# Kernel tuning notes

Measured on AMD Instinct MI355X. Metric: run time of the kernel, lower is better.

## Reference

```python
import jax, jax.numpy as jnp
import numpy as np

N_NEURONS = 256
P_MAX = 8
N_BLOCKS = P_MAX + 1
HIDDEN = 32
BATCH = 8192


def setup_inputs() -> dict:
    key = jax.random.key(0)
    ks = jax.random.split(key, 9)
    z = jax.random.normal(ks[0], (BATCH, N_BLOCKS * N_NEURONS), dtype=jnp.float32)
    # Per-block ScalarMLP params, stacked over the n_blocks axis.
    s1 = 1.0 / np.sqrt(N_NEURONS)
    s2 = 1.0 / np.sqrt(HIDDEN)
    gW1 = jax.random.uniform(ks[1], (N_BLOCKS, N_NEURONS, HIDDEN), jnp.float32, -s1, s1)
    gb1 = jax.random.uniform(ks[2], (N_BLOCKS, HIDDEN), jnp.float32, -s1, s1)
    gW2 = jax.random.uniform(ks[3], (N_BLOCKS, HIDDEN, HIDDEN), jnp.float32, -s2, s2)
    gb2 = jax.random.uniform(ks[4], (N_BLOCKS, HIDDEN), jnp.float32, -s2, s2)
    gW3 = jax.random.uniform(ks[5], (N_BLOCKS, HIDDEN), jnp.float32, -s2, s2)
    gb3 = jax.random.uniform(ks[6], (N_BLOCKS,), jnp.float32, -s2, s2)
    # Lag coupling matrices W_r ~ U(-init_scale, init_scale), init_scale=0.1
    W = jax.random.uniform(ks[7], (P_MAX, N_NEURONS, N_NEURONS), jnp.float32, -0.1, 0.1)
    return {"z": z, "gW1": gW1, "gb1": gb1, "gW2": gW2, "gb2": gb2,
            "gW3": gW3, "gb3": gb3, "W": W}


def _energy(z, gW1, gb1, gW2, gb2, gW3, gb3, W):
    B = z.shape[0]
    blocks = z.reshape(B, N_BLOCKS, N_NEURONS)           # (B, K, n)
    # Per-block ScalarMLP energies (all blocks at once).
    h1 = jax.nn.silu(jnp.einsum('bkn,knh->bkh', blocks, gW1) + gb1)   # (B, K, H)
    h2 = jax.nn.silu(jnp.einsum('bkh,khg->bkg', h1, gW2) + gb2)       # (B, K, H)
    e = jnp.einsum('bkh,kh->bk', h2, gW3) + gb3                        # (B, K)
    # Bilinear lag couplings: z_future^T W_r z_{lag-r}, r = 1..p_max.
    z_future = blocks[:, P_MAX, :]                                     # (B, n)
    lags = blocks[:, :P_MAX, :][:, ::-1, :]                            # (B, p, n), index r-1 == block p_max-r
    cross = jnp.einsum('bi,rij,brj->b', z_future, W, lags)             # (B,)
    return e.sum(axis=-1) + cross                                      # (B,)


def reference(z, gW1, gb1, gW2, gb2, gW3, gb3, W):
    # Score s(z) = -grad_z U(z); sum over batch gives per-sample grads
    # since energies are independent across samples.
    grad_z = jax.grad(lambda zz: _energy(zz, gW1, gb1, gW2, gb2, gW3, gb3, W).sum())(z)
    return -grad_z
```

## Files before the change

kernel.cpp:

```cpp
#include <hip/hip_runtime.h>
#include <hip/hip_bf16.h>
#include <math.h>

#define BATCH 8192
#define NB 9
#define NN 256
#define PMAX 8
#define HID 32
#define ZDIM 2304

typedef short bf16x8 __attribute__((ext_vector_type(8)));
typedef float f32x4 __attribute__((ext_vector_type(4)));

static __device__ inline unsigned short f2bf(float f) {
    __hip_bfloat16 h = __float2bfloat16(f);
    return *reinterpret_cast<unsigned short*>(&h);
}

static __device__ inline uint4 pack8(float4 a, float4 b) {
    uint4 u;
    u.x = (unsigned)f2bf(a.x) | ((unsigned)f2bf(a.y) << 16);
    u.y = (unsigned)f2bf(a.z) | ((unsigned)f2bf(a.w) << 16);
    u.z = (unsigned)f2bf(b.x) | ((unsigned)f2bf(b.y) << 16);
    u.w = (unsigned)f2bf(b.z) | ((unsigned)f2bf(b.w) << 16);
    return u;
}

__global__ __launch_bounds__(256) void k_pack(
    const float* __restrict__ W, const float* __restrict__ gW1,
    unsigned short* __restrict__ Wb, unsigned short* __restrict__ WTb,
    unsigned short* __restrict__ gW1b, unsigned short* __restrict__ g1Tb) {
    int r = blockIdx.z;
    int t = threadIdx.x;
    if (r < 8) {
        __shared__ float tt[32][33];
        int i0 = blockIdx.y * 32;
        int j0 = blockIdx.x * 32;
        int tx = t & 31;
        int ty = t >> 5;
        const float* src = W + (size_t)r * 65536;
        #pragma unroll
        for (int s = 0; s < 32; s += 8) {
            float v = src[(size_t)(i0 + ty + s) * 256 + (j0 + tx)];
            tt[ty + s][tx] = v;
            Wb[(size_t)r * 65536 + (size_t)(i0 + ty + s) * 256 + (j0 + tx)] = f2bf(v);
        }
        __syncthreads();
        #pragma unroll
        for (int s = 0; s < 32; s += 8)
            WTb[(size_t)r * 65536 + (size_t)(j0 + ty + s) * 256 + (i0 + tx)] = f2bf(tt[tx][ty + s]);
    } else {
        int tg = (blockIdx.y * 8 + blockIdx.x) * 256 + t;
        for (int e = tg; e < 73728; e += 16384) {
            float v = gW1[e];
            unsigned short b = f2bf(v);
            gW1b[e] = b;
            int k = e >> 13, n = (e >> 5) & 255, h = e & 31;
            g1Tb[(size_t)(k * 32 + h) * 256 + n] = b;
        }
    }
}

__global__ __launch_bounds__(256) void k_mlp(
    const float* __restrict__ z, const unsigned short* __restrict__ g1Tb,
    const float* __restrict__ gb1, const float* __restrict__ gW2,
    const float* __restrict__ gb2, const float* __restrict__ gW3,
    float* __restrict__ d1ws) {
    __shared__ uint4 As4[512];
    __shared__ uint4 Bw[1024];
    __shared__ uint4 W2Ts4[128];
    __shared__ uint4 W2Ns4[128];

    int t = threadIdx.x;
    int lane = t & 63;
    int w = t >> 6;
    int k = blockIdx.y;
    int b0 = blockIdx.x * 128;

    const unsigned short* bsrc = g1Tb + (size_t)k * 8192;
    for (int e = t; e < 1024; e += 256) {
        int h = e >> 5;
        int rest = e & 31;
        int c = rest >> 2, q = rest & 3;
        Bw[c * 128 + (h & 15) + 16 * q + 64 * (h >> 4)] =
            *(const uint4*)(bsrc + (size_t)h * 256 + c * 32 + q * 8);
    }
    const float* gw2 = gW2 + (size_t)k * 1024;
    unsigned short* w2t = (unsigned short*)W2Ts4;
    unsigned short* w2n = (unsigned short*)W2Ns4;
    for (int e = t; e < 1024; e += 256) {
        int n = e >> 5, kk = e & 31;
        int q = kk >> 3, jj = kk & 7;
        int ci = (n & 15) + 16 * q + 64 * (n >> 4);
        w2t[ci * 8 + jj] = f2bf(gw2[kk * 32 + n]);
        w2n[ci * 8 + jj] = f2bf(gw2[n * 32 + kk]);
    }

    int mq_m = t >> 2;
    int q = t & 3;

    f32x4 acc1[2][2];
    #pragma unroll
    for (int i = 0; i < 2; ++i)
        #pragma unroll
        for (int j = 0; j < 2; ++j) acc1[i][j] = (f32x4){0.f, 0.f, 0.f, 0.f};

    for (int c = 0; c < 8; ++c) {
        float4 fa[2][2];
        #pragma unroll
        for (int pp = 0; pp < 2; ++pp) {
            int m = mq_m + 64 * pp;
            const float* as = z + (size_t)(b0 + m) * ZDIM + k * 256 + c * 32 + q * 8;
            fa[pp][0] = *(const float4*)(as);
            fa[pp][1] = *(const float4*)(as + 4);
        }
        __syncthreads();
        #pragma unroll
        for (int pp = 0; pp < 2; ++pp) {
            int m = mq_m + 64 * pp;
            As4[(m & 15) + 16 * q + 64 * (m >> 4)] = pack8(fa[pp][0], fa[pp][1]);
        }
        __syncthreads();
        bf16x8 af[2], bfr[2];
        #pragma unroll
        for (int i = 0; i < 2; ++i) af[i] = __builtin_bit_cast(bf16x8, As4[lane + (w * 2 + i) * 64]);
        #pragma unroll
        for (int j = 0; j < 2; ++j) bfr[j] = __builtin_bit_cast(bf16x8, Bw[c * 128 + lane + j * 64]);
        #pragma unroll
        for (int i = 0; i < 2; ++i)
            #pragma unroll
            for (int j = 0; j < 2; ++j)
                acc1[i][j] = __builtin_amdgcn_mfma_f32_16x16x32_bf16(af[i], bfr[j], acc1[i][j], 0, 0, 0);
    }

    int cq = lane >> 4;
    int ci16 = lane & 15;
    float b1v[2], b2v[2], g3v[2];
    #pragma unroll
    for (int j = 0; j < 2; ++j) {
        b1v[j] = gb1[k * 32 + j * 16 + ci16];
        b2v[j] = gb2[k * 32 + j * 16 + ci16];
        g3v[j] = gW3[k * 32 + j * 16 + ci16];
    }
    unsigned short* Hs = (unsigned short*)As4;
    float sp1[2][2][4];
    __syncthreads();
    #pragma unroll
    for (int i = 0; i < 2; ++i)
        #pragma unroll
        for (int j = 0; j < 2; ++j)
            #pragma unroll
            for (int r = 0; r < 4; ++r) {
                float a1 = acc1[i][j][r] + b1v[j];
                float s1 = 1.f / (1.f + __expf(-a1));
                sp1[i][j][r] = s1 * (1.f + a1 * (1.f - s1));
                int row = w * 32 + i * 16 + cq * 4 + r;
                int col = j * 16 + ci16;
                int chunk = (row & 15) + 16 * (col >> 3) + 64 * (row >> 4);
                Hs[chunk * 8 + (col & 7)] = f2bf(a1 * s1);
            }
    __syncthreads();

    bf16x8 af2[2], wf[2];
    #pragma unroll
    for (int i = 0; i < 2; ++i) af2[i] = __builtin_bit_cast(bf16x8, As4[lane + (w * 2 + i) * 64]);
    #pragma unroll
    for (int j = 0; j < 2; ++j) wf[j] = __builtin_bit_cast(bf16x8, W2Ts4[lane + j * 64]);
    f32x4 acc2[2][2];
    #pragma unroll
    for (int i = 0; i < 2; ++i)
        #pragma unroll
        for (int j = 0; j < 2; ++j) {
            acc2[i][j] = (f32x4){0.f, 0.f, 0.f, 0.f};
            acc2[i][j] = __builtin_amdgcn_mfma_f32_16x16x32_bf16(af2[i], wf[j], acc2[i][j], 0, 0, 0);
        }

    __syncthreads();
    #pragma unroll
    for (int i = 0; i < 2; ++i)
        #pragma unroll
        for (int j = 0; j < 2; ++j)
            #pragma unroll
            for (int r = 0; r < 4; ++r) {
                float a2 = acc2[i][j][r] + b2v[j];
                float s2 = 1.f / (1.f + __expf(-a2));
                float da2 = g3v[j] * s2 * (1.f + a2 * (1.f - s2));
                int row = w * 32 + i * 16 + cq * 4 + r;
                int col = j * 16 + ci16;
                int chunk = (row & 15) + 16 * (col >> 3) + 64 * (row >> 4);
                Hs[chunk * 8 + (col & 7)] = f2bf(da2);
            }
    __syncthreads();

    bf16x8 af3[2], wg[2];
    #pragma unroll
    for (int i = 0; i < 2; ++i) af3[i] = __builtin_bit_cast(bf16x8, As4[lane + (w * 2 + i) * 64]);
    #pragma unroll
    for (int j = 0; j < 2; ++j) wg[j] = __builtin_bit_cast(bf16x8, W2Ns4[lane + j * 64]);
    #pragma unroll
    for (int i = 0; i < 2; ++i)
        #pragma unroll
        for (int j = 0; j < 2; ++j) {
            f32x4 a3 = (f32x4){0.f, 0.f, 0.f, 0.f};
            a3 = __builtin_amdgcn_mfma_f32_16x16x32_bf16(af3[i], wg[j], a3, 0, 0, 0);
            #pragma unroll
            for (int r = 0; r < 4; ++r) {
                int row = w * 32 + i * 16 + cq * 4 + r;
                int col = j * 16 + ci16;
                d1ws[((size_t)k * BATCH + b0 + row) * 32 + col] = a3[r] * sp1[i][j][r];
            }
        }
}

__global__ __launch_bounds__(256) void k_gemm_lo(
    const float* __restrict__ z, const float* __restrict__ d1,
    const unsigned short* __restrict__ WTb, const unsigned short* __restrict__ gW1b,
    float* __restrict__ out) {
    __shared__ uint4 As4[512];
    __shared__ uint4 Bs4[512];

    int t = threadIdx.x;
    int lane = t & 63;
    int w = t >> 6;
    int wr = w >> 1, wc = w & 1;
    int b0 = blockIdx.y * 128;
    int n0 = blockIdx.x * 128;
    int k  = n0 >> 8;
    int jb = n0 & 255;

    const float* Amain = z + (size_t)b0 * ZDIM + 2048;
    const float* Aext  = d1 + ((size_t)k * BATCH + b0) * 32;
    const unsigned short* Bmain = WTb + (size_t)(7 - k) * 65536 + (size_t)jb * 256;
    const unsigned short* Bext  = gW1b + ((size_t)k * 256 + jb) * 32;

    int mq_m = t >> 2;
    int q    = t & 3;

    f32x4 acc[4][4];
    #pragma unroll
    for (int i = 0; i < 4; ++i)
        #pragma unroll
        for (int j = 0; j < 4; ++j) acc[i][j] = (f32x4){0.f, 0.f, 0.f, 0.f};

    for (int c = 0; c < 9; ++c) {
        int kb = c * 32;
        float4 fa[2][2];
        uint4 bu[2];
        #pragma unroll
        for (int pp = 0; pp < 2; ++pp) {
            int m = mq_m + 64 * pp;
            const float* as = (c < 8) ? (Amain + (size_t)m * ZDIM + kb + q * 8)
                                      : (Aext + (size_t)m * 32 + q * 8);
            fa[pp][0] = *(const float4*)(as);
            fa[pp][1] = *(const float4*)(as + 4);
            const unsigned short* bs = (c < 8) ? (Bmain + (size_t)m * 256 + kb + q * 8)
                                               : (Bext + (size_t)m * 32 + q * 8);
            bu[pp] = *(const uint4*)(bs);
        }
        __syncthreads();
        #pragma unroll
        for (int pp = 0; pp < 2; ++pp) {
            int m = mq_m + 64 * pp;
            int ci = (m & 15) + 16 * q + 64 * (m >> 4);
            As4[ci] = pack8(fa[pp][0], fa[pp][1]);
            Bs4[ci] = bu[pp];
        }
        __syncthreads();
        bf16x8 af[4], bf[4];
        #pragma unroll
        for (int i = 0; i < 4; ++i) af[i] = __builtin_bit_cast(bf16x8, As4[lane + (wr * 4 + i) * 64]);
        #pragma unroll
        for (int j = 0; j < 4; ++j) bf[j] = __builtin_bit_cast(bf16x8, Bs4[lane + (wc * 4 + j) * 64]);
        #pragma unroll
        for (int i = 0; i < 4; ++i)
            #pragma unroll
            for (int j = 0; j < 4; ++j)
                acc[i][j] = __builtin_amdgcn_mfma_f32_16x16x32_bf16(af[i], bf[j], acc[i][j], 0, 0, 0);
    }

    int rquad = lane >> 4;
    int cidx  = lane & 15;
    #pragma unroll
    for (int i = 0; i < 4; ++i) {
        #pragma unroll
        for (int j = 0; j < 4; ++j) {
            float* o = out + (size_t)(b0 + wr * 64 + i * 16 + rquad * 4) * ZDIM
                     + (k * 256 + jb + wc * 64 + j * 16 + cidx);
            #pragma unroll
            for (int r = 0; r < 4; ++r)
                o[(size_t)r * ZDIM] = -acc[i][j][r];
        }
    }
}

__global__ __launch_bounds__(256) void k_gemm_hi(
    const float* __restrict__ z, const float* __restrict__ d1,
    const unsigned short* __restrict__ Wb, const unsigned short* __restrict__ gW1b,
    float* __restrict__ out) {
    __shared__ uint4 As4[512];
    __shared__ uint4 Bs4[256];

    int t = threadIdx.x;
    int lane = t & 63;
    int w = t >> 6;
    int b0 = blockIdx.y * 128;
    int i0 = blockIdx.x * 64;

    const float* Amain = z + (size_t)b0 * ZDIM;
    const float* Aext  = d1 + ((size_t)8 * BATCH + b0) * 32;
    const unsigned short* Bext = gW1b + (size_t)(8 * 256 + i0) * 32;

    int mq_m = t >> 2;
    int q    = t & 3;

    f32x4 acc[2][4];
    #pragma unroll
    for (int i = 0; i < 2; ++i)
        #pragma unroll
        for (int j = 0; j < 4; ++j) acc[i][j] = (f32x4){0.f, 0.f, 0.f, 0.f};

    for (int c = 0; c < 65; ++c) {
        int kb = c * 32;
        float4 fa[2][2];
        #pragma unroll
        for (int pp = 0; pp < 2; ++pp) {
            int m = mq_m + 64 * pp;
            const float* as = (c < 64) ? (Amain + (size_t)m * ZDIM + kb + q * 8)
                                       : (Aext + (size_t)m * 32 + q * 8);
            fa[pp][0] = *(const float4*)(as);
            fa[pp][1] = *(const float4*)(as + 4);
        }
        int bn = t >> 2;
        uint4 bu;
        if (c < 64) {
            int lag = c >> 3;
            int j0  = kb & 255;
            bu = *(const uint4*)(Wb + (size_t)(7 - lag) * 65536 + (size_t)(i0 + bn) * 256 + j0 + q * 8);
        } else {
            bu = *(const uint4*)(Bext + (size_t)bn * 32 + q * 8);
        }
        __syncthreads();
        #pragma unroll
        for (int pp = 0; pp < 2; ++pp) {
            int m = mq_m + 64 * pp;
            As4[(m & 15) + 16 * q + 64 * (m >> 4)] = pack8(fa[pp][0], fa[pp][1]);
        }
        Bs4[(bn & 15) + 16 * q + 64 * (bn >> 4)] = bu;
        __syncthreads();
        bf16x8 af[2], bf[4];
        #pragma unroll
        for (int i = 0; i < 2; ++i) af[i] = __builtin_bit_cast(bf16x8, As4[lane + (w * 2 + i) * 64]);
        #pragma unroll
        for (int j = 0; j < 4; ++j) bf[j] = __builtin_bit_cast(bf16x8, Bs4[lane + j * 64]);
        #pragma unroll
        for (int i = 0; i < 2; ++i)
            #pragma unroll
            for (int j = 0; j < 4; ++j)
                acc[i][j] = __builtin_amdgcn_mfma_f32_16x16x32_bf16(af[i], bf[j], acc[i][j], 0, 0, 0);
    }

    int rquad = lane >> 4;
    int cidx  = lane & 15;
    #pragma unroll
    for (int i = 0; i < 2; ++i) {
        #pragma unroll
        for (int j = 0; j < 4; ++j) {
            float* o = out + (size_t)(b0 + w * 32 + i * 16 + rquad * 4) * ZDIM
                     + (2048 + i0 + j * 16 + cidx);
            #pragma unroll
            for (int r = 0; r < 4; ++r)
                o[(size_t)r * ZDIM] = -acc[i][j][r];
        }
    }
}

extern "C" void kernel_launch(void* const* d_in, const int* in_sizes, int n_in,
                              void* d_out, int out_size, void* d_ws, size_t ws_size,
                              hipStream_t stream) {
    const float* z   = (const float*)d_in[0];
    const float* gW1 = (const float*)d_in[1];
    const float* gb1 = (const float*)d_in[2];
    const float* gW2 = (const float*)d_in[3];
    const float* gb2 = (const float*)d_in[4];
    const float* gW3 = (const float*)d_in[5];
    const float* W   = (const float*)d_in[7];
    float* out = (float*)d_out;

    float* ws = (float*)d_ws;
    float*          d1ws = ws;
    unsigned short* Wb   = (unsigned short*)(ws + 2359296);
    unsigned short* WTb  = Wb + 524288;
    unsigned short* gW1b = WTb + 524288;
    unsigned short* g1Tb = gW1b + 73728;

    k_pack<<<dim3(8, 8, 9), 256, 0, stream>>>(W, gW1, Wb, WTb, gW1b, g1Tb);
    k_mlp<<<dim3(64, 9), 256, 0, stream>>>(z, g1Tb, gb1, gW2, gb2, gW3, d1ws);
    k_gemm_lo<<<dim3(16, 64), 256, 0, stream>>>(z, d1ws, WTb, gW1b, out);
    k_gemm_hi<<<dim3(4, 64), 256, 0, stream>>>(z, d1ws, Wb, gW1b, out);
}
```

Before: 243.7 us.

## Merge cross GEMMs into one launch, prefetch tiles, store d1 as packed bf16

The two output GEMM kernels are merged into a single k_cross launch that dispatches on blockIdx.x: the first 4 columns compute the last block and the rest compute the lag blocks. Global loads for the next K-chunk are now issued after the shared-memory store, a register prefetch meant to overlap memory latency with MFMA work. k_mlp writes d1 as pre-swizzled bf16 tiles instead of fp32, which halves that traffic and lets the consumer copy tiles straight into LDS without conversion. Thread-to-row mapping is also changed so LDS stores are linear. This removes one launch and the fp32 d1 round trip, at the cost of more register pressure and branch divergence between the two block roles.

```diff
diff --git a/kernel.cpp b/kernel.cpp
--- a/kernel.cpp
+++ b/kernel.cpp
@@ -65,7 +65,7 @@
     const float* __restrict__ z, const unsigned short* __restrict__ g1Tb,
     const float* __restrict__ gb1, const float* __restrict__ gW2,
     const float* __restrict__ gb2, const float* __restrict__ gW3,
-    float* __restrict__ d1ws) {
+    uint4* __restrict__ d1b) {
     __shared__ uint4 As4[512];
     __shared__ uint4 Bw[1024];
     __shared__ uint4 W2Ts4[128];
@@ -75,30 +75,38 @@
     int lane = t & 63;
     int w = t >> 6;
     int k = blockIdx.y;
-    int b0 = blockIdx.x * 128;
+    int bx = blockIdx.x;
+    int b0 = bx * 128;
 
     const unsigned short* bsrc = g1Tb + (size_t)k * 8192;
     for (int e = t; e < 1024; e += 256) {
-        int h = e >> 5;
-        int rest = e & 31;
-        int c = rest >> 2, q = rest & 3;
-        Bw[c * 128 + (h & 15) + 16 * q + 64 * (h >> 4)] =
-            *(const uint4*)(bsrc + (size_t)h * 256 + c * 32 + q * 8);
+        int c = e >> 7, rest = e & 127;
+        int h = (rest & 15) + ((rest >> 6) << 4);
+        int q2 = (rest >> 4) & 3;
+        Bw[e] = *(const uint4*)(bsrc + (size_t)h * 256 + c * 32 + q2 * 8);
     }
     const float* gw2 = gW2 + (size_t)k * 1024;
     unsigned short* w2t = (unsigned short*)W2Ts4;
     unsigned short* w2n = (unsigned short*)W2Ns4;
     for (int e = t; e < 1024; e += 256) {
         int n = e >> 5, kk = e & 31;
-        int q = kk >> 3, jj = kk & 7;
-        int ci = (n & 15) + 16 * q + 64 * (n >> 4);
+        int q2 = kk >> 3, jj = kk & 7;
+        int ci = (n & 15) + 16 * q2 + 64 * (n >> 4);
         w2t[ci * 8 + jj] = f2bf(gw2[kk * 32 + n]);
         w2n[ci * 8 + jj] = f2bf(gw2[n * 32 + kk]);
     }
 
-    int mq_m = t >> 2;
-    int q = t & 3;
-
+    int m_lin = (t & 15) + ((t >> 6) << 4);
+    int q = (t >> 4) & 3;
+    const float* zbase = z + (size_t)b0 * ZDIM + k * 256 + q * 8;
+
+    float4 fa[2][2];
+    #pragma unroll
+    for (int pp = 0; pp < 2; ++pp) {
+        const float* p = zbase + (size_t)(m_lin + 64 * pp) * ZDIM;
+        fa[pp][0] = ((const float4*)p)[0];
+        fa[pp][1] = ((const float4*)p)[1];
+    }
     f32x4 acc1[2][2];
     #pragma unroll
     for (int i = 0; i < 2; ++i)
@@ -106,21 +114,19 @@
         for (int j = 0; j < 2; ++j) acc1[i][j] = (f32x4){0.f, 0.f, 0.f, 0.f};
 
     for (int c = 0; c < 8; ++c) {
-        float4 fa[2][2];
-        #pragma unroll
-        for (int pp = 0; pp < 2; ++pp) {
-            int m = mq_m + 64 * pp;
-            const float* as = z + (size_t)(b0 + m) * ZDIM + k * 256 + c * 32 + q * 8;
-            fa[pp][0] = *(const float4*)(as);
-            fa[pp][1] = *(const float4*)(as + 4);
-        }
         __syncthreads();
         #pragma unroll
-        for (int pp = 0; pp < 2; ++pp) {
-            int m = mq_m + 64 * pp;
-            As4[(m & 15) + 16 * q + 64 * (m >> 4)] = pack8(fa[pp][0], fa[pp][1]);
-        }
+        for (int pp = 0; pp < 2; ++pp)
+            As4[256 * pp + t] = pack8(fa[pp][0], fa[pp][1]);
         __syncthreads();
+        if (c < 7) {
+            #pragma unroll
+            for (int pp = 0; pp < 2; ++pp) {
+                const float* p = zbase + (size_t)(m_lin + 64 * pp) * ZDIM + (c + 1) * 32;
+                fa[pp][0] = ((const float4*)p)[0];
+                fa[pp][1] = ((const float4*)p)[1];
+            }
+        }
         bf16x8 af[2], bfr[2];
         #pragma unroll
         for (int i = 0; i < 2; ++i) af[i] = __builtin_bit_cast(bf16x8, As4[lane + (w * 2 + i) * 64]);
@@ -197,6 +203,7 @@
     for (int i = 0; i < 2; ++i) af3[i] = __builtin_bit_cast(bf16x8, As4[lane + (w * 2 + i) * 64]);
     #pragma unroll
     for (int j = 0; j < 2; ++j) wg[j] = __builtin_bit_cast(bf16x8, W2Ns4[lane + j * 64]);
+    float d1v[2][2][4];
     #pragma unroll
     for (int i = 0; i < 2; ++i)
         #pragma unroll
@@ -204,173 +211,189 @@
             f32x4 a3 = (f32x4){0.f, 0.f, 0.f, 0.f};
             a3 = __builtin_amdgcn_mfma_f32_16x16x32_bf16(af3[i], wg[j], a3, 0, 0, 0);
             #pragma unroll
+            for (int r = 0; r < 4; ++r) d1v[i][j][r] = a3[r] * sp1[i][j][r];
+        }
+    __syncthreads();
+    #pragma unroll
+    for (int i = 0; i < 2; ++i)
+        #pragma unroll
+        for (int j = 0; j < 2; ++j)
+            #pragma unroll
             for (int r = 0; r < 4; ++r) {
                 int row = w * 32 + i * 16 + cq * 4 + r;
                 int col = j * 16 + ci16;
-                d1ws[((size_t)k * BATCH + b0 + row) * 32 + col] = a3[r] * sp1[i][j][r];
-            }
-        }
-}
-
-__global__ __launch_bounds__(256) void k_gemm_lo(
-    const float* __restrict__ z, const float* __restrict__ d1,
-    const unsigned short* __restrict__ WTb, const unsigned short* __restrict__ gW1b,
-    float* __restrict__ out) {
+                int chunk = (row & 15) + 16 * (col >> 3) + 64 * (row >> 4);
+                Hs[chunk * 8 + (col & 7)] = f2bf(d1v[i][j][r]);
+            }
+    __syncthreads();
+    uint4* dst = d1b + ((size_t)k * 64 + bx) * 512;
+    #pragma unroll
+    for (int pp = 0; pp < 2; ++pp)
+        dst[256 * pp + t] = As4[256 * pp + t];
+}
+
+__global__ __launch_bounds__(256) void k_cross(
+    const float* __restrict__ z, const uint4* __restrict__ d1b,
+    const unsigned short* __restrict__ Wb, const unsigned short* __restrict__ WTb,
+    const unsigned short* __restrict__ gW1b, float* __restrict__ out) {
     __shared__ uint4 As4[512];
     __shared__ uint4 Bs4[512];
 
     int t = threadIdx.x;
     int lane = t & 63;
     int w = t >> 6;
-    int wr = w >> 1, wc = w & 1;
-    int b0 = blockIdx.y * 128;
-    int n0 = blockIdx.x * 128;
-    int k  = n0 >> 8;
-    int jb = n0 & 255;
-
-    const float* Amain = z + (size_t)b0 * ZDIM + 2048;
-    const float* Aext  = d1 + ((size_t)k * BATCH + b0) * 32;
-    const unsigned short* Bmain = WTb + (size_t)(7 - k) * 65536 + (size_t)jb * 256;
-    const unsigned short* Bext  = gW1b + ((size_t)k * 256 + jb) * 32;
-
-    int mq_m = t >> 2;
-    int q    = t & 3;
-
-    f32x4 acc[4][4];
-    #pragma unroll
-    for (int i = 0; i < 4; ++i)
-        #pragma unroll
-        for (int j = 0; j < 4; ++j) acc[i][j] = (f32x4){0.f, 0.f, 0.f, 0.f};
-
-    for (int c = 0; c < 9; ++c) {
-        int kb = c * 32;
+    int by = blockIdx.y;
+    int b0 = by * 128;
+    int bx = blockIdx.x;
+    int m_lin = (t & 15) + ((t >> 6) << 4);
+    int q = (t >> 4) & 3;
+    int rquad = lane >> 4;
+    int cidx = lane & 15;
+
+    if (bx >= 4) {
+        int kb_ = bx - 4;
+        int k = kb_ >> 1, jb = (kb_ & 1) * 128;
+        const float* Az = z + (size_t)b0 * ZDIM + 2048 + q * 8;
+        const uint4* Ad = d1b + ((size_t)k * 64 + by) * 512;
+        const unsigned short* Bm = WTb + (size_t)(7 - k) * 65536 + (size_t)jb * 256 + q * 8;
+        const unsigned short* Be = gW1b + ((size_t)k * 256 + jb) * 32 + q * 8;
+        int wr = w >> 1, wc = w & 1;
+
         float4 fa[2][2];
-        uint4 bu[2];
+        uint4 au[2], bu[2];
         #pragma unroll
         for (int pp = 0; pp < 2; ++pp) {
-            int m = mq_m + 64 * pp;
-            const float* as = (c < 8) ? (Amain + (size_t)m * ZDIM + kb + q * 8)
-                                      : (Aext + (size_t)m * 32 + q * 8);
-            fa[pp][0] = *(const float4*)(as);
-            fa[pp][1] = *(const float4*)(as + 4);
-            const unsigned short* bs = (c < 8) ? (Bmain + (size_t)m * 256 + kb + q * 8)
-                                               : (Bext + (size_t)m * 32 + q * 8);
-            bu[pp] = *(const uint4*)(bs);
-        }
-        __syncthreads();
+            const float* p = Az + (size_t)(m_lin + 64 * pp) * ZDIM;
+            fa[pp][0] = ((const float4*)p)[0];
+            fa[pp][1] = ((const float4*)p)[1];
+            bu[pp] = *(const uint4*)(Bm + (size_t)(m_lin + 64 * pp) * 256);
+        }
+        f32x4 acc[4][4];
+        #pragma unroll
+        for (int i = 0; i < 4; ++i)
+            #pragma unroll
+            for (int j = 0; j < 4; ++j) acc[i][j] = (f32x4){0.f, 0.f, 0.f, 0.f};
+
+        for (int c = 0; c < 9; ++c) {
+            bool tail = (c == 8);
+            __syncthreads();
+            #pragma unroll
+            for (int pp = 0; pp < 2; ++pp) {
+                As4[256 * pp + t] = tail ? au[pp] : pack8(fa[pp][0], fa[pp][1]);
+                Bs4[256 * pp + t] = bu[pp];
+            }
+            __syncthreads();
+            if (c < 8) {
+                int cn = c + 1;
+                if (cn < 8) {
+                    #pragma unroll
+                    for (int pp = 0; pp < 2; ++pp) {
+                        const float* p = Az + (size_t)(m_lin + 64 * pp) * ZDIM + cn * 32;
+                        fa[pp][0] = ((const float4*)p)[0];
+                        fa[pp][1] = ((const float4*)p)[1];
+                        bu[pp] = *(const uint4*)(Bm + (size_t)(m_lin + 64 * pp) * 256 + cn * 32);
+                    }
+                } else {
+                    #pragma unroll
+                    for (int pp = 0; pp < 2; ++pp) {
+                        au[pp] = Ad[256 * pp + t];
+                        bu[pp] = *(const uint4*)(Be + (size_t)(m_lin + 64 * pp) * 32);
+                    }
+                }
+            }
+            bf16x8 af[4], bf[4];
+            #pragma unroll
+            for (int i = 0; i < 4; ++i) af[i] = __builtin_bit_cast(bf16x8, As4[lane + (wr * 4 + i) * 64]);
+            #pragma unroll
+            for (int j = 0; j < 4; ++j) bf[j] = __builtin_bit_cast(bf16x8, Bs4[lane + (wc * 4 + j) * 64]);
+            #pragma unroll
+            for (int i = 0; i < 4; ++i)
+                #pragma unroll
+                for (int j = 0; j < 4; ++j)
+                    acc[i][j] = __builtin_amdgcn_mfma_f32_16x16x32_bf16(af[i], bf[j], acc[i][j], 0, 0, 0);
+        }
+        #pragma unroll
+        for (int i = 0; i < 4; ++i)
+            #pragma unroll
+            for (int j = 0; j < 4; ++j) {
+                float* o = out + (size_t)(b0 + wr * 64 + i * 16 + rquad * 4) * ZDIM
+                         + (k * 256 + jb + wc * 64 + j * 16 + cidx);
+                #pragma unroll
+                for (int r = 0; r < 4; ++r)
+                    o[(size_t)r * ZDIM] = -acc[i][j][r];
+            }
+    } else {
+        int i0 = bx * 64;
+        const float* Az = z + (size_t)b0 * ZDIM + q * 8;
+        const uint4* Ad = d1b + ((size_t)8 * 64 + by) * 512;
+        const unsigned short* Be = gW1b + (size_t)(8 * 256 + i0) * 32 + q * 8;
+        int bn = m_lin;
+
+        float4 fa[2][2];
+        uint4 au[2], bu;
         #pragma unroll
         for (int pp = 0; pp < 2; ++pp) {
-            int m = mq_m + 64 * pp;
-            int ci = (m & 15) + 16 * q + 64 * (m >> 4);
-            As4[ci] = pack8(fa[pp][0], fa[pp][1]);
-            Bs4[ci] = bu[pp];
-        }
-        __syncthreads();
-        bf16x8 af[4], bf[4];
-        #pragma unroll
-        for (int i = 0; i < 4; ++i) af[i] = __builtin_bit_cast(bf16x8, As4[lane + (wr * 4 + i) * 64]);
-        #pragma unroll
-        for (int j = 0; j < 4; ++j) bf[j] = __builtin_bit_cast(bf16x8, Bs4[lane + (wc * 4 + j) * 64]);
-        #pragma unroll
-        for (int i = 0; i < 4; ++i)
-            #pragma unroll
-            for (int j = 0; j < 4; ++j)
-                acc[i][j] = __builtin_amdgcn_mfma_f32_16x16x32_bf16(af[i], bf[j], acc[i][j], 0, 0, 0);
-    }
-
-    int rquad = lane >> 4;
-    int cidx  = lane & 15;
-    #pragma unroll
-    for (int i = 0; i < 4; ++i) {
-        #pragma unroll
-        for (int j = 0; j < 4; ++j) {
-            float* o = out + (size_t)(b0 + wr * 64 + i * 16 + rquad * 4) * ZDIM
-                     + (k * 256 + jb + wc * 64 + j * 16 + cidx);
-            #pragma unroll
-            for (int r = 0; r < 4; ++r)
-                o[(size_t)r * ZDIM] = -acc[i][j][r];
-        }
-    }
-}
-
-__global__ __launch_bounds__(256) void k_gemm_hi(
-    const float* __restrict__ z, const float* __restrict__ d1,
-    const unsigned short* __restrict__ Wb, const unsigned short* __restrict__ gW1b,
-    float* __restrict__ out) {
-    __shared__ uint4 As4[512];
-    __shared__ uint4 Bs4[256];
-
-    int t = threadIdx.x;
-    int lane = t & 63;
-    int w = t >> 6;
-    int b0 = blockIdx.y * 128;
-    int i0 = blockIdx.x * 64;
-
-    const float* Amain = z + (size_t)b0 * ZDIM;
-    const float* Aext  = d1 + ((size_t)8 * BATCH + b0) * 32;
-    const unsigned short* Bext = gW1b + (size_t)(8 * 256 + i0) * 32;
-
-    int mq_m = t >> 2;
-    int q    = t & 3;
-
-    f32x4 acc[2][4];
-    #pragma unroll
-    for (int i = 0; i < 2; ++i)
-        #pragma unroll
-        for (int j = 0; j < 4; ++j) acc[i][j] = (f32x4){0.f, 0.f, 0.f, 0.f};
-
-    for (int c = 0; c < 65; ++c) {
-        int kb = c * 32;
-        float4 fa[2][2];
-        #pragma unroll
-        for (int pp = 0; pp < 2; ++pp) {
-            int m = mq_m + 64 * pp;
-            const float* as = (c < 64) ? (Amain + (size_t)m * ZDIM + kb + q * 8)
-                                       : (Aext + (size_t)m * 32 + q * 8);
-            fa[pp][0] = *(const float4*)(as);
-            fa[pp][1] = *(const float4*)(as + 4);
-        }
-        int bn = t >> 2;
-        uint4 bu;
-        if (c < 64) {
-            int lag = c >> 3;
-            int j0  = kb & 255;
-            bu = *(const uint4*)(Wb + (size_t)(7 - lag) * 65536 + (size_t)(i0 + bn) * 256 + j0 + q * 8);
-        } else {
-            bu = *(const uint4*)(Bext + (size_t)bn * 32 + q * 8);
-        }
-        __syncthreads();
-        #pragma unroll
-        for (int pp = 0; pp < 2; ++pp) {
-            int m = mq_m + 64 * pp;
-            As4[(m & 15) + 16 * q + 64 * (m >> 4)] = pack8(fa[pp][0], fa[pp][1]);
-        }
-        Bs4[(bn & 15) + 16 * q + 64 * (bn >> 4)] = bu;
-        __syncthreads();
-        bf16x8 af[2], bf[4];
-        #pragma unroll
-        for (int i = 0; i < 2; ++i) af[i] = __builtin_bit_cast(bf16x8, As4[lane + (w * 2 + i) * 64]);
-        #pragma unroll
-        for (int j = 0; j < 4; ++j) bf[j] = __builtin_bit_cast(bf16x8, Bs4[lane + j * 64]);
+            const float* p = Az + (size_t)(m_lin + 64 * pp) * ZDIM;
+            fa[pp][0] = ((const float4*)p)[0];
+            fa[pp][1] = ((const float4*)p)[1];
+        }
+        bu = *(const uint4*)(Wb + (size_t)7 * 65536 + (size_t)(i0 + bn) * 256 + q * 8);
+
+        f32x4 acc[2][4];
         #pragma unroll
         for (int i = 0; i < 2; ++i)
             #pragma unroll
-            for (int j = 0; j < 4; ++j)
-                acc[i][j] = __builtin_amdgcn_mfma_f32_16x16x32_bf16(af[i], bf[j], acc[i][j], 0, 0, 0);
-    }
-
-    int rquad = lane >> 4;
-    int cidx  = lane & 15;
-    #pragma unroll
-    for (int i = 0; i < 2; ++i) {
-        #pragma unroll
-        for (int j = 0; j < 4; ++j) {
-            float* o = out + (size_t)(b0 + w * 32 + i * 16 + rquad * 4) * ZDIM
-                     + (2048 + i0 + j * 16 + cidx);
-            #pragma unroll
-            for (int r = 0; r < 4; ++r)
-                o[(size_t)r * ZDIM] = -acc[i][j][r];
-        }
+            for (int j = 0; j < 4; ++j) acc[i][j] = (f32x4){0.f, 0.f, 0.f, 0.f};
+
+        for (int c = 0; c < 65; ++c) {
+            bool tail = (c == 64);
+            __syncthreads();
+            #pragma unroll
+            for (int pp = 0; pp < 2; ++pp)
+                As4[256 * pp + t] = tail ? au[pp] : pack8(fa[pp][0], fa[pp][1]);
+            Bs4[t] = bu;
+            __syncthreads();
+            if (c < 64) {
+                int cn = c + 1;
+                if (cn < 64) {
+                    int kb = cn * 32;
+                    #pragma unroll
+                    for (int pp = 0; pp < 2; ++pp) {
+                        const float* p = Az + (size_t)(m_lin + 64 * pp) * ZDIM + kb;
+                        fa[pp][0] = ((const float4*)p)[0];
+                        fa[pp][1] = ((const float4*)p)[1];
+                    }
+                    int lag = cn >> 3;
+                    int j0 = kb & 255;
+                    bu = *(const uint4*)(Wb + (size_t)(7 - lag) * 65536
+                                         + (size_t)(i0 + bn) * 256 + j0 + q * 8);
+                } else {
+                    #pragma unroll
+                    for (int pp = 0; pp < 2; ++pp) au[pp] = Ad[256 * pp + t];
+                    bu = *(const uint4*)(Be + (size_t)bn * 32);
+                }
+            }
+            bf16x8 af[2], bf[4];
+            #pragma unroll
+            for (int i = 0; i < 2; ++i) af[i] = __builtin_bit_cast(bf16x8, As4[lane + (w * 2 + i) * 64]);
+            #pragma unroll
+            for (int j = 0; j < 4; ++j) bf[j] = __builtin_bit_cast(bf16x8, Bs4[lane + j * 64]);
+            #pragma unroll
+            for (int i = 0; i < 2; ++i)
+                #pragma unroll
+                for (int j = 0; j < 4; ++j)
+                    acc[i][j] = __builtin_amdgcn_mfma_f32_16x16x32_bf16(af[i], bf[j], acc[i][j], 0, 0, 0);
+        }
+        #pragma unroll
+        for (int i = 0; i < 2; ++i)
+            #pragma unroll
+            for (int j = 0; j < 4; ++j) {
+                float* o = out + (size_t)(b0 + w * 32 + i * 16 + rquad * 4) * ZDIM
+                         + (2048 + i0 + j * 16 + cidx);
+                #pragma unroll
+                for (int r = 0; r < 4; ++r)
+                    o[(size_t)r * ZDIM] = -acc[i][j][r];
+            }
     }
 }
 
@@ -386,15 +409,14 @@
     const float* W   = (const float*)d_in[7];
     float* out = (float*)d_out;
 
-    float* ws = (float*)d_ws;
-    float*          d1ws = ws;
-    unsigned short* Wb   = (unsigned short*)(ws + 2359296);
+    char* ws = (char*)d_ws;
+    uint4*          d1b  = (uint4*)ws;
+    unsigned short* Wb   = (unsigned short*)(ws + 4718592);
     unsigned short* WTb  = Wb + 524288;
     unsigned short* gW1b = WTb + 524288;
     unsigned short* g1Tb = gW1b + 73728;
 
     k_pack<<<dim3(8, 8, 9), 256, 0, stream>>>(W, gW1, Wb, WTb, gW1b, g1Tb);
-    k_mlp<<<dim3(64, 9), 256, 0, stream>>>(z, g1Tb, gb1, gW2, gb2, gW3, d1ws);
-    k_gemm_lo<<<dim3(16, 64), 256, 0, stream>>>(z, d1ws, WTb, gW1b, out);
-    k_gemm_hi<<<dim3(4, 64), 256, 0, stream>>>(z, d1ws, Wb, gW1b, out);
-}
+    k_mlp<<<dim3(64, 9), 256, 0, stream>>>(z, g1Tb, gb1, gW2, gb2, gW3, d1b);
+    k_cross<<<dim3(20, 64), 256, 0, stream>>>(z, d1b, Wb, WTb, gW1b, out);
+}
```

Result: slower. 282.8 us (+16.0%).
